# Kernel tuning notes

Hardware: AMD Instinct MI355X
Metric: run time of the kernel (lower is better)

## Reference

```python
import jax, jax.numpy as jnp
import numpy as np

# The 16 differentiable binary logic gates used by difflogic are all of the form
# c0 + c1*a + c2*b + c3*(a*b). Rows are gate ids 0..15.
GATE_COEF = jnp.array([
    [0., 0., 0., 0.],    # 0: False
    [0., 0., 0., 1.],    # 1: a AND b
    [0., 1., 0., -1.],   # 2: a AND NOT b
    [0., 1., 0., 0.],    # 3: a
    [0., 0., 1., -1.],   # 4: NOT a AND b
    [0., 0., 1., 0.],    # 5: b
    [0., 1., 1., -2.],   # 6: XOR
    [0., 1., 1., -1.],   # 7: OR
    [1., -1., -1., 1.],  # 8: NOR
    [1., -1., -1., 2.],  # 9: XNOR
    [1., 0., -1., 0.],   # 10: NOT b
    [1., 0., -1., 1.],   # 11: a OR NOT b (b implies a)
    [1., -1., 0., 0.],   # 12: NOT a
    [1., -1., 0., 1.],   # 13: NOT a OR b (a implies b)
    [1., 0., 0., -1.],   # 14: NAND
    [1., 0., 0., 0.],    # 15: True
], dtype=jnp.float32)

BATCH = 256
IN_DIM = 1024
WIDTH = 64000
K = 10
TAU = 30.0


def _logic_layer(x, w, idx_a, idx_b):
    # x: [B, in_dim], w: [out, 16], idx_*: [out] int32
    a = x[:, idx_a]            # [B, out]
    b = x[:, idx_b]            # [B, out]
    coef = jax.nn.softmax(w, axis=-1) @ GATE_COEF   # [out, 4]
    return coef[:, 0] + coef[:, 1] * a + coef[:, 2] * b + coef[:, 3] * (a * b)


def setup_inputs() -> dict:
    key = jax.random.key(0)
    ks = jax.random.split(key, 10)
    x = jax.random.uniform(ks[0], (BATCH, IN_DIM), dtype=jnp.float32)
    w1 = jax.random.normal(ks[1], (WIDTH, 16), dtype=jnp.float32)
    w2 = jax.random.normal(ks[2], (WIDTH, 16), dtype=jnp.float32)
    w3 = jax.random.normal(ks[3], (WIDTH, 16), dtype=jnp.float32)
    idx_a1 = jax.random.randint(ks[4], (WIDTH,), 0, IN_DIM, dtype=jnp.int32)
    idx_b1 = jax.random.randint(ks[5], (WIDTH,), 0, IN_DIM, dtype=jnp.int32)
    idx_a2 = jax.random.randint(ks[6], (WIDTH,), 0, WIDTH, dtype=jnp.int32)
    idx_b2 = jax.random.randint(ks[7], (WIDTH,), 0, WIDTH, dtype=jnp.int32)
    idx_a3 = jax.random.randint(ks[8], (WIDTH,), 0, WIDTH, dtype=jnp.int32)
    idx_b3 = jax.random.randint(ks[9], (WIDTH,), 0, WIDTH, dtype=jnp.int32)
    return {"x": x, "w1": w1, "w2": w2, "w3": w3,
            "idx_a1": idx_a1, "idx_b1": idx_b1,
            "idx_a2": idx_a2, "idx_b2": idx_b2,
            "idx_a3": idx_a3, "idx_b3": idx_b3}


def reference(x, w1, w2, w3, idx_a1, idx_b1, idx_a2, idx_b2, idx_a3, idx_b3):
    h = _logic_layer(x, w1, idx_a1, idx_b1)
    h = _logic_layer(h, w2, idx_a2, idx_b2)
    h = _logic_layer(h, w3, idx_a3, idx_b3)
    # GroupSum: [B, WIDTH] -> [B, K, WIDTH//K] -> sum -> / tau
    return h.reshape(h.shape[0], K, -1).sum(axis=-1) / TAU
```

## Files before the change

### kernel.cpp

```cpp
#include <hip/hip_runtime.h>
#include <stdint.h>


#define BATCH   256
#define IN_DIM  1024
#define WIDTH   64000
#define NGROUP  10
#define GSIZE   6400
#define TAU     30.0f
#define NWAVE   16
#define GPW     8
#define GPB     (NWAVE*GPW)
#define NBLK    (WIDTH/GPB)

typedef unsigned short ushort_t;

static __device__ __forceinline__ float bf2f(ushort_t s) {
    return __uint_as_float((uint32_t)s << 16);
}
static __device__ __forceinline__ ushort_t f2bf(float f) {
    uint32_t u = __float_as_uint(f);
    return (ushort_t)((u + 0x7fffu + ((u >> 16) & 1u)) >> 16);
}
static __device__ __forceinline__ float4 up4(ushort4 s) {
    return make_float4(bf2f(s.x), bf2f(s.y), bf2f(s.z), bf2f(s.w));
}
static __device__ __forceinline__ float4 gate4(float4 c, float4 a, float4 b) {
    float4 r;
    r.x = fmaf(c.w, a.x * b.x, fmaf(c.z, b.x, fmaf(c.y, a.x, c.x)));
    r.y = fmaf(c.w, a.y * b.y, fmaf(c.z, b.y, fmaf(c.y, a.y, c.x)));
    r.z = fmaf(c.w, a.z * b.z, fmaf(c.z, b.z, fmaf(c.y, a.z, c.x)));
    r.w = fmaf(c.w, a.w * b.w, fmaf(c.z, b.w, fmaf(c.y, a.w, c.x)));
    return r;
}

__global__ __launch_bounds__(256) void transpose_kernel(
    const float* __restrict__ x, ushort_t* __restrict__ xT)
{
    __shared__ float tile[64][65];
    const int c0 = (blockIdx.x & 15) * 64;
    const int b0 = (blockIdx.x >> 4) * 64;
    const int lt = threadIdx.x & 63;
    const int wt = threadIdx.x >> 6;
    for (int r = wt; r < 64; r += 4)
        tile[r][lt] = x[(b0 + r) * IN_DIM + c0 + lt];
    __syncthreads();
    for (int r = wt; r < 64; r += 4)
        xT[(c0 + r) * BATCH + b0 + lt] = f2bf(tile[lt][r]);
}

__global__ __launch_bounds__(256) void coef_kernel(
    const float* __restrict__ w1, const float* __restrict__ w2,
    const float* __restrict__ w3,
    float4* __restrict__ c1o, float4* __restrict__ c2o, float4* __restrict__ c3o)
{
    const int id = blockIdx.x * 256 + threadIdx.x;
    const int layer = id / WIDTH;
    const int j = id - layer * WIDTH;
    const float* w = (layer == 0) ? w1 : (layer == 1) ? w2 : w3;
    float4* cc     = (layer == 0) ? c1o : (layer == 1) ? c2o : c3o;

    const float4* w4 = (const float4*)(w + (size_t)j * 16);
    float4 q0 = w4[0], q1 = w4[1], q2 = w4[2], q3 = w4[3];
    float p[16] = {q0.x,q0.y,q0.z,q0.w, q1.x,q1.y,q1.z,q1.w,
                   q2.x,q2.y,q2.z,q2.w, q3.x,q3.y,q3.z,q3.w};
    float m = p[0];
    #pragma unroll
    for (int i = 1; i < 16; ++i) m = fmaxf(m, p[i]);
    float s = 0.f;
    #pragma unroll
    for (int i = 0; i < 16; ++i) { p[i] = __expf(p[i] - m); s += p[i]; }
    const float inv = 1.0f / s;

    float c0 = (p[8]+p[9]+p[10]+p[11]+p[12]+p[13]+p[14]+p[15]) * inv;
    float c1 = (p[2]+p[3]+p[6]+p[7] - p[8]-p[9]-p[12]-p[13]) * inv;
    float c2 = (p[4]+p[5]+p[6]+p[7] - p[8]-p[9]-p[10]-p[11]) * inv;
    float c3 = (p[1]-p[2]-p[4]-2.f*p[6]-p[7]+p[8]+2.f*p[9]+p[11]+p[13]-p[14]) * inv;
    cc[j] = make_float4(c0, c1, c2, c3);
}

__global__ __launch_bounds__(256) void prep_kernel(
    const int* __restrict__ ia1, const int* __restrict__ ib1,
    const int* __restrict__ ia2, const int* __restrict__ ib2,
    const int* __restrict__ ia3, const int* __restrict__ ib3,
    const float4* __restrict__ c1, const float4* __restrict__ c2,
    const float4* __restrict__ c3,
    int* __restrict__ leaf,
    float4* __restrict__ pc)
{
    const int j = blockIdx.x * 256 + threadIdx.x;
    if (j >= WIDTH) return;

    const int pa = ia3[j], pb = ib3[j];
    const int qaa = ia2[pa], qab = ib2[pa];
    const int qba = ia2[pb], qbb = ib2[pb];

    int* L = leaf + (size_t)j * 8;
    L[0] = ia1[qaa]; L[1] = ib1[qaa];
    L[2] = ia1[qab]; L[3] = ib1[qab];
    L[4] = ia1[qba]; L[5] = ib1[qba];
    L[6] = ia1[qbb]; L[7] = ib1[qbb];

    float4* P = pc + (size_t)j * 7;
    P[0] = c1[qaa]; P[1] = c1[qab]; P[2] = c1[qba]; P[3] = c1[qbb];
    P[4] = c2[pa];  P[5] = c2[pb];
    P[6] = c3[j];
}

__global__ __launch_bounds__(1024) void fused_kernel(
    const ushort_t* __restrict__ xT,
    const int*      __restrict__ leaf,
    const float4*   __restrict__ pc,
    float*          __restrict__ red_out)
{
    const int lane = threadIdx.x & 63;
    const int wave = __builtin_amdgcn_readfirstlane(threadIdx.x >> 6);
    const int jw = blockIdx.x * GPB + wave * GPW;

    float4 acc = make_float4(0.f, 0.f, 0.f, 0.f);

    #pragma unroll 2
    for (int u = 0; u < GPW; ++u) {
        const int j = jw + u;
        const int* Lp = leaf + (size_t)j * 8;
        const int l0 = __builtin_amdgcn_readfirstlane(Lp[0]);
        const int l1 = __builtin_amdgcn_readfirstlane(Lp[1]);
        const int l2 = __builtin_amdgcn_readfirstlane(Lp[2]);
        const int l3 = __builtin_amdgcn_readfirstlane(Lp[3]);
        const int l4 = __builtin_amdgcn_readfirstlane(Lp[4]);
        const int l5 = __builtin_amdgcn_readfirstlane(Lp[5]);
        const int l6 = __builtin_amdgcn_readfirstlane(Lp[6]);
        const int l7 = __builtin_amdgcn_readfirstlane(Lp[7]);

        const ushort4 v0 = ((const ushort4*)(xT + (size_t)l0 * BATCH))[lane];
        const ushort4 v1 = ((const ushort4*)(xT + (size_t)l1 * BATCH))[lane];
        const ushort4 v2 = ((const ushort4*)(xT + (size_t)l2 * BATCH))[lane];
        const ushort4 v3 = ((const ushort4*)(xT + (size_t)l3 * BATCH))[lane];
        const ushort4 v4 = ((const ushort4*)(xT + (size_t)l4 * BATCH))[lane];
        const ushort4 v5 = ((const ushort4*)(xT + (size_t)l5 * BATCH))[lane];
        const ushort4 v6 = ((const ushort4*)(xT + (size_t)l6 * BATCH))[lane];
        const ushort4 v7 = ((const ushort4*)(xT + (size_t)l7 * BATCH))[lane];

        const float4* Pp = pc + (size_t)j * 7;
        const float4 C1aa = Pp[0], C1ab = Pp[1], C1ba = Pp[2], C1bb = Pp[3];
        const float4 C2a  = Pp[4], C2b  = Pp[5], C3c = Pp[6];

        const float4 haa = gate4(C1aa, up4(v0), up4(v1));
        const float4 hab = gate4(C1ab, up4(v2), up4(v3));
        const float4 hba = gate4(C1ba, up4(v4), up4(v5));
        const float4 hbb = gate4(C1bb, up4(v6), up4(v7));
        const float4 h2a = gate4(C2a, haa, hab);
        const float4 h2b = gate4(C2b, hba, hbb);
        const float4 h3  = gate4(C3c, h2a, h2b);
        acc.x += h3.x; acc.y += h3.y; acc.z += h3.z; acc.w += h3.w;
    }

    __shared__ float4 s[NWAVE][64];
    s[wave][lane] = acc;
    __syncthreads();
    if (wave == 0) {
        float4 t = s[0][lane];
        #pragma unroll
        for (int w = 1; w < NWAVE; ++w) {
            float4 q = s[w][lane];
            t.x += q.x; t.y += q.y; t.z += q.z; t.w += q.w;
        }
        const float sc = 1.0f / TAU;
        const int grp = (blockIdx.x * GPB) / GSIZE;
        const int b0 = lane * 4;
        atomicAdd(&red_out[(b0 + 0) * NGROUP + grp], t.x * sc);
        atomicAdd(&red_out[(b0 + 1) * NGROUP + grp], t.y * sc);
        atomicAdd(&red_out[(b0 + 2) * NGROUP + grp], t.z * sc);
        atomicAdd(&red_out[(b0 + 3) * NGROUP + grp], t.w * sc);
    }
}

extern "C" void kernel_launch(void* const* d_in, const int* in_sizes, int n_in,
                              void* d_out, int out_size, void* d_ws, size_t ws_size,
                              hipStream_t stream)
{
    const float* x   = (const float*)d_in[0];
    const float* w1  = (const float*)d_in[1];
    const float* w2  = (const float*)d_in[2];
    const float* w3  = (const float*)d_in[3];
    const int*   ia1 = (const int*)d_in[4];
    const int*   ib1 = (const int*)d_in[5];
    const int*   ia2 = (const int*)d_in[6];
    const int*   ib2 = (const int*)d_in[7];
    const int*   ia3 = (const int*)d_in[8];
    const int*   ib3 = (const int*)d_in[9];
    float* out = (float*)d_out;

    char* ws = (char*)d_ws;
    ushort_t* xT = (ushort_t*)ws;
    float*    c1 = (float*)(ws + (size_t)IN_DIM * BATCH * 2);
    float*    c2 = c1 + (size_t)WIDTH * 4;
    float*    c3 = c2 + (size_t)WIDTH * 4;
    int*    leaf = (int*)(c3 + (size_t)WIDTH * 4);
    float4*   pc = (float4*)(leaf + (size_t)WIDTH * 8);

    hipMemsetAsync(d_out, 0, (size_t)out_size * sizeof(float), stream);

    transpose_kernel<<<64, 256, 0, stream>>>(x, xT);
    coef_kernel<<<(3 * WIDTH) / 256, 256, 0, stream>>>(w1, w2, w3,
                                                       (float4*)c1, (float4*)c2, (float4*)c3);
    prep_kernel<<<WIDTH / 256, 256, 0, stream>>>(ia1, ib1, ia2, ib2, ia3, ib3,
                                                 (const float4*)c1, (const float4*)c2,
                                                 (const float4*)c3, leaf, pc);
    fused_kernel<<<NBLK, 1024, 0, stream>>>(xT, leaf, pc, out);
}
```

Measured before the change: 135.0 us.

## Fuse softmax coefficients into prep kernel and stage tree params in LDS

```diff
diff --git a/kernel.cpp b/kernel.cpp
--- a/kernel.cpp
+++ b/kernel.cpp
@@ -22,16 +22,19 @@
     uint32_t u = __float_as_uint(f);
     return (ushort_t)((u + 0x7fffu + ((u >> 16) & 1u)) >> 16);
 }
+static __device__ __forceinline__ float gate1(float4 c, float a, float b) {
+    return fmaf(b, fmaf(c.w, a, c.z), fmaf(c.y, a, c.x));
+}
+static __device__ __forceinline__ float4 gate4(float4 c, float4 a, float4 b) {
+    float4 r;
+    r.x = gate1(c, a.x, b.x);
+    r.y = gate1(c, a.y, b.y);
+    r.z = gate1(c, a.z, b.z);
+    r.w = gate1(c, a.w, b.w);
+    return r;
+}
 static __device__ __forceinline__ float4 up4(ushort4 s) {
     return make_float4(bf2f(s.x), bf2f(s.y), bf2f(s.z), bf2f(s.w));
-}
-static __device__ __forceinline__ float4 gate4(float4 c, float4 a, float4 b) {
-    float4 r;
-    r.x = fmaf(c.w, a.x * b.x, fmaf(c.z, b.x, fmaf(c.y, a.x, c.x)));
-    r.y = fmaf(c.w, a.y * b.y, fmaf(c.z, b.y, fmaf(c.y, a.y, c.x)));
-    r.z = fmaf(c.w, a.z * b.z, fmaf(c.z, b.z, fmaf(c.y, a.z, c.x)));
-    r.w = fmaf(c.w, a.w * b.w, fmaf(c.z, b.w, fmaf(c.y, a.w, c.x)));
-    return r;
 }
 
 __global__ __launch_bounds__(256) void transpose_kernel(
@@ -49,18 +52,9 @@
         xT[(c0 + r) * BATCH + b0 + lt] = f2bf(tile[lt][r]);
 }
 
-__global__ __launch_bounds__(256) void coef_kernel(
-    const float* __restrict__ w1, const float* __restrict__ w2,
-    const float* __restrict__ w3,
-    float4* __restrict__ c1o, float4* __restrict__ c2o, float4* __restrict__ c3o)
-{
-    const int id = blockIdx.x * 256 + threadIdx.x;
-    const int layer = id / WIDTH;
-    const int j = id - layer * WIDTH;
-    const float* w = (layer == 0) ? w1 : (layer == 1) ? w2 : w3;
-    float4* cc     = (layer == 0) ? c1o : (layer == 1) ? c2o : c3o;
-
-    const float4* w4 = (const float4*)(w + (size_t)j * 16);
+static __device__ __forceinline__ float4 softmax_coef(const float* __restrict__ w)
+{
+    const float4* w4 = (const float4*)w;
     float4 q0 = w4[0], q1 = w4[1], q2 = w4[2], q3 = w4[3];
     float p[16] = {q0.x,q0.y,q0.z,q0.w, q1.x,q1.y,q1.z,q1.w,
                    q2.x,q2.y,q2.z,q2.w, q3.x,q3.y,q3.z,q3.w};
@@ -71,20 +65,19 @@
     #pragma unroll
     for (int i = 0; i < 16; ++i) { p[i] = __expf(p[i] - m); s += p[i]; }
     const float inv = 1.0f / s;
-
     float c0 = (p[8]+p[9]+p[10]+p[11]+p[12]+p[13]+p[14]+p[15]) * inv;
     float c1 = (p[2]+p[3]+p[6]+p[7] - p[8]-p[9]-p[12]-p[13]) * inv;
     float c2 = (p[4]+p[5]+p[6]+p[7] - p[8]-p[9]-p[10]-p[11]) * inv;
     float c3 = (p[1]-p[2]-p[4]-2.f*p[6]-p[7]+p[8]+2.f*p[9]+p[11]+p[13]-p[14]) * inv;
-    cc[j] = make_float4(c0, c1, c2, c3);
+    return make_float4(c0, c1, c2, c3);
 }
 
 __global__ __launch_bounds__(256) void prep_kernel(
+    const float* __restrict__ w1, const float* __restrict__ w2,
+    const float* __restrict__ w3,
     const int* __restrict__ ia1, const int* __restrict__ ib1,
     const int* __restrict__ ia2, const int* __restrict__ ib2,
     const int* __restrict__ ia3, const int* __restrict__ ib3,
-    const float4* __restrict__ c1, const float4* __restrict__ c2,
-    const float4* __restrict__ c3,
     int* __restrict__ leaf,
     float4* __restrict__ pc)
 {
@@ -102,9 +95,13 @@
     L[6] = ia1[qbb]; L[7] = ib1[qbb];
 
     float4* P = pc + (size_t)j * 7;
-    P[0] = c1[qaa]; P[1] = c1[qab]; P[2] = c1[qba]; P[3] = c1[qbb];
-    P[4] = c2[pa];  P[5] = c2[pb];
-    P[6] = c3[j];
+    P[0] = softmax_coef(w1 + (size_t)qaa * 16);
+    P[1] = softmax_coef(w1 + (size_t)qab * 16);
+    P[2] = softmax_coef(w1 + (size_t)qba * 16);
+    P[3] = softmax_coef(w1 + (size_t)qbb * 16);
+    P[4] = softmax_coef(w2 + (size_t)pa * 16);
+    P[5] = softmax_coef(w2 + (size_t)pb * 16);
+    P[6] = softmax_coef(w3 + (size_t)j * 16);
 }
 
 __global__ __launch_bounds__(1024) void fused_kernel(
@@ -113,24 +110,34 @@
     const float4*   __restrict__ pc,
     float*          __restrict__ red_out)
 {
-    const int lane = threadIdx.x & 63;
-    const int wave = __builtin_amdgcn_readfirstlane(threadIdx.x >> 6);
-    const int jw = blockIdx.x * GPB + wave * GPW;
+    __shared__ int    sleaf[GPB * 8];
+    __shared__ float4 spc[GPB * 7];
+    __shared__ float4 sred[NWAVE][64];
+
+    const int tid = threadIdx.x;
+
+    sleaf[tid] = leaf[(size_t)blockIdx.x * (GPB * 8) + tid];
+    if (tid < GPB * 7)
+        spc[tid] = pc[(size_t)blockIdx.x * (GPB * 7) + tid];
+    __syncthreads();
+
+    const int lane = tid & 63;
+    const int wave = tid >> 6;
+    const int gbase = wave * GPW;
 
     float4 acc = make_float4(0.f, 0.f, 0.f, 0.f);
 
-    #pragma unroll 2
+    #pragma unroll
     for (int u = 0; u < GPW; ++u) {
-        const int j = jw + u;
-        const int* Lp = leaf + (size_t)j * 8;
-        const int l0 = __builtin_amdgcn_readfirstlane(Lp[0]);
-        const int l1 = __builtin_amdgcn_readfirstlane(Lp[1]);
-        const int l2 = __builtin_amdgcn_readfirstlane(Lp[2]);
-        const int l3 = __builtin_amdgcn_readfirstlane(Lp[3]);
-        const int l4 = __builtin_amdgcn_readfirstlane(Lp[4]);
-        const int l5 = __builtin_amdgcn_readfirstlane(Lp[5]);
-        const int l6 = __builtin_amdgcn_readfirstlane(Lp[6]);
-        const int l7 = __builtin_amdgcn_readfirstlane(Lp[7]);
+        const int g = gbase + u;
+        const int l0 = __builtin_amdgcn_readfirstlane(sleaf[g*8 + 0]);
+        const int l1 = __builtin_amdgcn_readfirstlane(sleaf[g*8 + 1]);
+        const int l2 = __builtin_amdgcn_readfirstlane(sleaf[g*8 + 2]);
+        const int l3 = __builtin_amdgcn_readfirstlane(sleaf[g*8 + 3]);
+        const int l4 = __builtin_amdgcn_readfirstlane(sleaf[g*8 + 4]);
+        const int l5 = __builtin_amdgcn_readfirstlane(sleaf[g*8 + 5]);
+        const int l6 = __builtin_amdgcn_readfirstlane(sleaf[g*8 + 6]);
+        const int l7 = __builtin_amdgcn_readfirstlane(sleaf[g*8 + 7]);
 
         const ushort4 v0 = ((const ushort4*)(xT + (size_t)l0 * BATCH))[lane];
         const ushort4 v1 = ((const ushort4*)(xT + (size_t)l1 * BATCH))[lane];
@@ -141,9 +148,13 @@
         const ushort4 v6 = ((const ushort4*)(xT + (size_t)l6 * BATCH))[lane];
         const ushort4 v7 = ((const ushort4*)(xT + (size_t)l7 * BATCH))[lane];
 
-        const float4* Pp = pc + (size_t)j * 7;
-        const float4 C1aa = Pp[0], C1ab = Pp[1], C1ba = Pp[2], C1bb = Pp[3];
-        const float4 C2a  = Pp[4], C2b  = Pp[5], C3c = Pp[6];
+        const float4 C1aa = spc[g*7 + 0];
+        const float4 C1ab = spc[g*7 + 1];
+        const float4 C1ba = spc[g*7 + 2];
+        const float4 C1bb = spc[g*7 + 3];
+        const float4 C2a  = spc[g*7 + 4];
+        const float4 C2b  = spc[g*7 + 5];
+        const float4 C3c  = spc[g*7 + 6];
 
         const float4 haa = gate4(C1aa, up4(v0), up4(v1));
         const float4 hab = gate4(C1ab, up4(v2), up4(v3));
@@ -155,14 +166,13 @@
         acc.x += h3.x; acc.y += h3.y; acc.z += h3.z; acc.w += h3.w;
     }
 
-    __shared__ float4 s[NWAVE][64];
-    s[wave][lane] = acc;
+    sred[wave][lane] = acc;
     __syncthreads();
     if (wave == 0) {
-        float4 t = s[0][lane];
+        float4 t = sred[0][lane];
         #pragma unroll
         for (int w = 1; w < NWAVE; ++w) {
-            float4 q = s[w][lane];
+            float4 q = sred[w][lane];
             t.x += q.x; t.y += q.y; t.z += q.z; t.w += q.w;
         }
         const float sc = 1.0f / TAU;
@@ -193,19 +203,14 @@
 
     char* ws = (char*)d_ws;
     ushort_t* xT = (ushort_t*)ws;
-    float*    c1 = (float*)(ws + (size_t)IN_DIM * BATCH * 2);
-    float*    c2 = c1 + (size_t)WIDTH * 4;
-    float*    c3 = c2 + (size_t)WIDTH * 4;
-    int*    leaf = (int*)(c3 + (size_t)WIDTH * 4);
+    int*    leaf = (int*)(ws + (size_t)IN_DIM * BATCH * 2);
     float4*   pc = (float4*)(leaf + (size_t)WIDTH * 8);
 
     hipMemsetAsync(d_out, 0, (size_t)out_size * sizeof(float), stream);
 
     transpose_kernel<<<64, 256, 0, stream>>>(x, xT);
-    coef_kernel<<<(3 * WIDTH) / 256, 256, 0, stream>>>(w1, w2, w3,
-                                                       (float4*)c1, (float4*)c2, (float4*)c3);
-    prep_kernel<<<WIDTH / 256, 256, 0, stream>>>(ia1, ib1, ia2, ib2, ia3, ib3,
-                                                 (const float4*)c1, (const float4*)c2,
-                                                 (const float4*)c3, leaf, pc);
+    prep_kernel<<<WIDTH / 256, 256, 0, stream>>>(w1, w2, w3,
+                                                 ia1, ib1, ia2, ib2, ia3, ib3,
+                                                 leaf, pc);
     fused_kernel<<<NBLK, 1024, 0, stream>>>(xT, leaf, pc, out);
 }
```

Result: slower. 378.7 us (+180.5%).

## Stage batch-sliced input table in LDS and gather leaves from shared memory

Applied to the files above, without the earlier changes.

```diff
diff --git a/kernel.cpp b/kernel.cpp
--- a/kernel.cpp
+++ b/kernel.cpp
@@ -8,30 +8,25 @@
 #define NGROUP  10
 #define GSIZE   6400
 #define TAU     30.0f
-#define NWAVE   16
-#define GPW     8
-#define GPB     (NWAVE*GPW)
-#define NBLK    (WIDTH/GPB)
+#define NWAVE   8
+#define SLICES  4
+#define SB      64
+#define GPB2    512
+#define NCHUNK  (WIDTH/GPB2)
+#define MCH     128
+#define NBLK    (NCHUNK*SLICES)
 
 typedef unsigned short ushort_t;
 
-static __device__ __forceinline__ float bf2f(ushort_t s) {
-    return __uint_as_float((uint32_t)s << 16);
-}
 static __device__ __forceinline__ ushort_t f2bf(float f) {
     uint32_t u = __float_as_uint(f);
     return (ushort_t)((u + 0x7fffu + ((u >> 16) & 1u)) >> 16);
 }
-static __device__ __forceinline__ float4 up4(ushort4 s) {
-    return make_float4(bf2f(s.x), bf2f(s.y), bf2f(s.z), bf2f(s.w));
-}
-static __device__ __forceinline__ float4 gate4(float4 c, float4 a, float4 b) {
-    float4 r;
-    r.x = fmaf(c.w, a.x * b.x, fmaf(c.z, b.x, fmaf(c.y, a.x, c.x)));
-    r.y = fmaf(c.w, a.y * b.y, fmaf(c.z, b.y, fmaf(c.y, a.y, c.x)));
-    r.z = fmaf(c.w, a.z * b.z, fmaf(c.z, b.z, fmaf(c.y, a.z, c.x)));
-    r.w = fmaf(c.w, a.w * b.w, fmaf(c.z, b.w, fmaf(c.y, a.w, c.x)));
-    return r;
+static __device__ __forceinline__ float bfu(ushort_t s) {
+    return __uint_as_float((uint32_t)s << 16);
+}
+static __device__ __forceinline__ float gate1(float4 c, float a, float b) {
+    return fmaf(b, fmaf(c.w, a, c.z), fmaf(c.y, a, c.x));
 }
 
 __global__ __launch_bounds__(256) void transpose_kernel(
@@ -71,7 +66,6 @@
     #pragma unroll
     for (int i = 0; i < 16; ++i) { p[i] = __expf(p[i] - m); s += p[i]; }
     const float inv = 1.0f / s;
-
     float c0 = (p[8]+p[9]+p[10]+p[11]+p[12]+p[13]+p[14]+p[15]) * inv;
     float c1 = (p[2]+p[3]+p[6]+p[7] - p[8]-p[9]-p[12]-p[13]) * inv;
     float c2 = (p[4]+p[5]+p[6]+p[7] - p[8]-p[9]-p[10]-p[11]) * inv;
@@ -107,71 +101,97 @@
     P[6] = c3[j];
 }
 
-__global__ __launch_bounds__(1024) void fused_kernel(
+__global__ __launch_bounds__(512) void fused_kernel(
     const ushort_t* __restrict__ xT,
     const int*      __restrict__ leaf,
     const float4*   __restrict__ pc,
     float*          __restrict__ red_out)
 {
-    const int lane = threadIdx.x & 63;
-    const int wave = __builtin_amdgcn_readfirstlane(threadIdx.x >> 6);
-    const int jw = blockIdx.x * GPB + wave * GPW;
-
-    float4 acc = make_float4(0.f, 0.f, 0.f, 0.f);
-
-    #pragma unroll 2
-    for (int u = 0; u < GPW; ++u) {
-        const int j = jw + u;
-        const int* Lp = leaf + (size_t)j * 8;
-        const int l0 = __builtin_amdgcn_readfirstlane(Lp[0]);
-        const int l1 = __builtin_amdgcn_readfirstlane(Lp[1]);
-        const int l2 = __builtin_amdgcn_readfirstlane(Lp[2]);
-        const int l3 = __builtin_amdgcn_readfirstlane(Lp[3]);
-        const int l4 = __builtin_amdgcn_readfirstlane(Lp[4]);
-        const int l5 = __builtin_amdgcn_readfirstlane(Lp[5]);
-        const int l6 = __builtin_amdgcn_readfirstlane(Lp[6]);
-        const int l7 = __builtin_amdgcn_readfirstlane(Lp[7]);
-
-        const ushort4 v0 = ((const ushort4*)(xT + (size_t)l0 * BATCH))[lane];
-        const ushort4 v1 = ((const ushort4*)(xT + (size_t)l1 * BATCH))[lane];
-        const ushort4 v2 = ((const ushort4*)(xT + (size_t)l2 * BATCH))[lane];
-        const ushort4 v3 = ((const ushort4*)(xT + (size_t)l3 * BATCH))[lane];
-        const ushort4 v4 = ((const ushort4*)(xT + (size_t)l4 * BATCH))[lane];
-        const ushort4 v5 = ((const ushort4*)(xT + (size_t)l5 * BATCH))[lane];
-        const ushort4 v6 = ((const ushort4*)(xT + (size_t)l6 * BATCH))[lane];
-        const ushort4 v7 = ((const ushort4*)(xT + (size_t)l7 * BATCH))[lane];
-
-        const float4* Pp = pc + (size_t)j * 7;
-        const float4 C1aa = Pp[0], C1ab = Pp[1], C1ba = Pp[2], C1bb = Pp[3];
-        const float4 C2a  = Pp[4], C2b  = Pp[5], C3c = Pp[6];
-
-        const float4 haa = gate4(C1aa, up4(v0), up4(v1));
-        const float4 hab = gate4(C1ab, up4(v2), up4(v3));
-        const float4 hba = gate4(C1ba, up4(v4), up4(v5));
-        const float4 hbb = gate4(C1bb, up4(v6), up4(v7));
-        const float4 h2a = gate4(C2a, haa, hab);
-        const float4 h2b = gate4(C2b, hba, hbb);
-        const float4 h3  = gate4(C3c, h2a, h2b);
-        acc.x += h3.x; acc.y += h3.y; acc.z += h3.z; acc.w += h3.w;
+    __shared__ ushort_t xs[IN_DIM * SB];
+    __shared__ int      sml[MCH * 8];
+    __shared__ float4   smc[MCH * 7];
+    __shared__ float2   sred[NWAVE][64];
+
+    const int tid   = threadIdx.x;
+    const int lane  = tid & 63;
+    const int wave  = tid >> 6;
+    const int chunk = blockIdx.x >> 2;
+    const int slice = blockIdx.x & 3;
+
+    {
+        const int sub = tid & 15;
+        const int r0  = tid >> 4;
+        for (int p = 0; p < 32; ++p) {
+            const int row = p * 32 + r0;
+            const uint2 v = *(const uint2*)(xT + (size_t)row * BATCH + slice * SB + sub * 4);
+            *(uint2*)(xs + row * SB + sub * 4) = v;
+        }
     }
 
-    __shared__ float4 s[NWAVE][64];
-    s[wave][lane] = acc;
+    const int gate0 = chunk * GPB2;
+    const int grp0  = gate0 / GSIZE;
+    const int split = (grp0 + 1) * GSIZE - gate0;
+
+    float acc0 = 0.f, acc1 = 0.f;
+
+    for (int ci = 0; ci < GPB2 / MCH; ++ci) {
+        __syncthreads();
+        const size_t mb = (size_t)(gate0 + ci * MCH);
+        ((int2*)sml)[tid] = ((const int2*)(leaf + mb * 8))[tid];
+        smc[tid] = pc[mb * 7 + tid];
+        if (tid < MCH * 7 - 512)
+            smc[512 + tid] = pc[mb * 7 + 512 + tid];
+        __syncthreads();
+
+        const int gw = wave * (MCH / NWAVE);
+        #pragma unroll 2
+        for (int i = 0; i < MCH / NWAVE; ++i) {
+            const int g = gw + i;
+            const int c0 = __builtin_amdgcn_readfirstlane(sml[g*8 + 0]);
+            const int c1 = __builtin_amdgcn_readfirstlane(sml[g*8 + 1]);
+            const int c2 = __builtin_amdgcn_readfirstlane(sml[g*8 + 2]);
+            const int c3 = __builtin_amdgcn_readfirstlane(sml[g*8 + 3]);
+            const int c4 = __builtin_amdgcn_readfirstlane(sml[g*8 + 4]);
+            const int c5 = __builtin_amdgcn_readfirstlane(sml[g*8 + 5]);
+            const int c6 = __builtin_amdgcn_readfirstlane(sml[g*8 + 6]);
+            const int c7 = __builtin_amdgcn_readfirstlane(sml[g*8 + 7]);
+
+            const float v0 = bfu(xs[c0 * SB + lane]);
+            const float v1 = bfu(xs[c1 * SB + lane]);
+            const float v2 = bfu(xs[c2 * SB + lane]);
+            const float v3 = bfu(xs[c3 * SB + lane]);
+            const float v4 = bfu(xs[c4 * SB + lane]);
+            const float v5 = bfu(xs[c5 * SB + lane]);
+            const float v6 = bfu(xs[c6 * SB + lane]);
+            const float v7 = bfu(xs[c7 * SB + lane]);
+
+            const float haa = gate1(smc[g*7 + 0], v0, v1);
+            const float hab = gate1(smc[g*7 + 1], v2, v3);
+            const float hba = gate1(smc[g*7 + 2], v4, v5);
+            const float hbb = gate1(smc[g*7 + 3], v6, v7);
+            const float h2a = gate1(smc[g*7 + 4], haa, hab);
+            const float h2b = gate1(smc[g*7 + 5], hba, hbb);
+            const float h3  = gate1(smc[g*7 + 6], h2a, h2b);
+
+            const int gl = ci * MCH + g;
+            if (gl < split) acc0 += h3; else acc1 += h3;
+        }
+    }
+
+    sred[wave][lane] = make_float2(acc0, acc1);
     __syncthreads();
     if (wave == 0) {
-        float4 t = s[0][lane];
+        float t0 = 0.f, t1 = 0.f;
         #pragma unroll
-        for (int w = 1; w < NWAVE; ++w) {
-            float4 q = s[w][lane];
-            t.x += q.x; t.y += q.y; t.z += q.z; t.w += q.w;
+        for (int w = 0; w < NWAVE; ++w) {
+            const float2 q = sred[w][lane];
+            t0 += q.x; t1 += q.y;
         }
         const float sc = 1.0f / TAU;
-        const int grp = (blockIdx.x * GPB) / GSIZE;
-        const int b0 = lane * 4;
-        atomicAdd(&red_out[(b0 + 0) * NGROUP + grp], t.x * sc);
-        atomicAdd(&red_out[(b0 + 1) * NGROUP + grp], t.y * sc);
-        atomicAdd(&red_out[(b0 + 2) * NGROUP + grp], t.z * sc);
-        atomicAdd(&red_out[(b0 + 3) * NGROUP + grp], t.w * sc);
+        const int b = slice * SB + lane;
+        atomicAdd(&red_out[b * NGROUP + grp0], t0 * sc);
+        if (split < GPB2)
+            atomicAdd(&red_out[b * NGROUP + grp0 + 1], t1 * sc);
     }
 }
 
@@ -193,19 +213,17 @@
 
     char* ws = (char*)d_ws;
     ushort_t* xT = (ushort_t*)ws;
-    float*    c1 = (float*)(ws + (size_t)IN_DIM * BATCH * 2);
-    float*    c2 = c1 + (size_t)WIDTH * 4;
-    float*    c3 = c2 + (size_t)WIDTH * 4;
-    int*    leaf = (int*)(c3 + (size_t)WIDTH * 4);
+    int*    leaf = (int*)(ws + (size_t)IN_DIM * BATCH * 2);
     float4*   pc = (float4*)(leaf + (size_t)WIDTH * 8);
+    float4*   c1 = pc + (size_t)WIDTH * 7;
+    float4*   c2 = c1 + WIDTH;
+    float4*   c3 = c2 + WIDTH;
 
     hipMemsetAsync(d_out, 0, (size_t)out_size * sizeof(float), stream);
 
     transpose_kernel<<<64, 256, 0, stream>>>(x, xT);
-    coef_kernel<<<(3 * WIDTH) / 256, 256, 0, stream>>>(w1, w2, w3,
-                                                       (float4*)c1, (float4*)c2, (float4*)c3);
+    coef_kernel<<<(3 * WIDTH) / 256, 256, 0, stream>>>(w1, w2, w3, c1, c2, c3);
     prep_kernel<<<WIDTH / 256, 256, 0, stream>>>(ia1, ib1, ia2, ib2, ia3, ib3,
-                                                 (const float4*)c1, (const float4*)c2,
-                                                 (const float4*)c3, leaf, pc);
-    fused_kernel<<<NBLK, 1024, 0, stream>>>(xT, leaf, pc, out);
-}
+                                                 c1, c2, c3, leaf, pc);
+    fused_kernel<<<NBLK, 512, 0, stream>>>(xT, leaf, pc, out);
+}
```

New measurement: 152.1 us. +12.7%, slower.
